# Kernel optimization log

Hardware: AMD Instinct MI355X
Metric: run time of the kernel (lower is better)

## Reference

```python
import jax, jax.numpy as jnp
import numpy as np

DIM = 640
M_SPATIAL = 100  # 10*10
BATCH = 64
EPS = 1e-5


def setup_inputs() -> dict:
    key = jax.random.key(0)
    kx, = jax.random.split(key, 1)
    x = jax.random.normal(kx, (BATCH, DIM, M_SPATIAL), dtype=jnp.float32)
    # temperature buffer: log(1 / (2 * H * W)) as in BDC.__init__
    t = jnp.log(1.0 / (2.0 * M_SPATIAL) * jnp.ones((1, 1), dtype=jnp.float32))
    return {"x": x, "t": t}


def reference(x, t):
    B, dim, M = x.shape
    # x_pow2 = x @ x^T  -> [B, dim, dim]
    x_pow2 = jnp.einsum('bim,bjm->bij', x, x)
    # I_M.bmm(x_pow2*I) broadcasts diag along rows; (x_pow2*I).bmm(I_M) along cols
    d = jnp.diagonal(x_pow2, axis1=1, axis2=2)  # [B, dim], squared norms
    dcov = d[:, :, None] + d[:, None, :] - 2.0 * x_pow2
    dcov = jnp.clip(dcov, 0.0)
    dcov = jnp.exp(t) * dcov
    dcov = jnp.sqrt(dcov + EPS)
    # double centering: dcov.bmm(I_M) = row sums broadcast, I_M.bmm(dcov) = col sums
    row_mean = jnp.sum(dcov, axis=2, keepdims=True) / dim          # [B, dim, 1]
    col_mean = jnp.sum(dcov, axis=1, keepdims=True) / dim          # [B, 1, dim]
    grand_mean = jnp.sum(dcov, axis=(1, 2), keepdims=True) / (dim * dim)
    bdc = dcov - row_mean - col_mean + grand_mean                   # [B, dim, dim]
    # Triuvec: upper triangle incl. diagonal, row-major order
    iu_r, iu_c = np.triu_indices(dim)
    return bdc[:, iu_r, iu_c]  # [B, dim*(dim+1)//2]
```

## Files before the change

kernel.cpp:

```cpp
#include <hip/hip_runtime.h>
#include <math.h>

#define BATCH 64
#define DIM   640
#define MSP   100
#define TILE  64
#define NT    10
#define NPAIR 55
#define PTRI  205120
#define EPSV  1e-5f

#define WS_D 0
#define WS_S 40960
#define WS_G 81920
#define XB_OFF 327936ull


typedef __attribute__((ext_vector_type(8))) short short8;
typedef __attribute__((ext_vector_type(4))) float f32x4;

__device__ __forceinline__ short f2bf(float f) {
    union { float f; unsigned u; } x; x.f = f;
    unsigned r = x.u + 0x7fffu + ((x.u >> 16) & 1u);
    return (short)(r >> 16);
}
__device__ __forceinline__ float bf2f(short h) {
    union { unsigned u; float f; } x; x.u = ((unsigned)(unsigned short)h) << 16;
    return x.f;
}

__device__ __forceinline__ void decode_pair(int u, int& ti, int& tj) {
    ti = 0;
    while (u >= NT - ti) { u -= NT - ti; ++ti; }
    tj = ti + u;
}

__device__ __forceinline__ void decode_block(int bid, int& b, int& ti, int& tj) {
    const int xcd = bid & 7;
    const int idx = bid >> 3;
    b = xcd + 8 * (idx & 7);
    decode_pair(idx >> 3, ti, tj);
}

__global__ __launch_bounds__(256) void k_prep(const float* __restrict__ x,
                                              float* __restrict__ ws) {
    short* xb = (short*)((char*)ws + XB_OFF);
    const int t = threadIdx.x;
    const int rr = t >> 4, c = t & 15;
    const int row = blockIdx.x * 16 + rr;
    const int k0 = c * 8;
    const float* src = x + (size_t)row * MSP;

    float v[8];
#pragma unroll
    for (int e = 0; e < 8; ++e) v[e] = 0.f;
    if (k0 <= 88) {
        float4 u0 = *(const float4*)(src + k0);
        float4 u1 = *(const float4*)(src + k0 + 4);
        v[0] = u0.x; v[1] = u0.y; v[2] = u0.z; v[3] = u0.w;
        v[4] = u1.x; v[5] = u1.y; v[6] = u1.z; v[7] = u1.w;
    } else if (k0 == 96) {
        float4 u0 = *(const float4*)(src + 96);
        v[0] = u0.x; v[1] = u0.y; v[2] = u0.z; v[3] = u0.w;
    }

    short8 h; float s = 0.f;
#pragma unroll
    for (int e = 0; e < 8; ++e) {
        short hb = f2bf(v[e]);
        float vr = bf2f(hb);
        s += vr * vr;
        h[e] = hb;
    }
    *(short8*)(xb + (size_t)blockIdx.x * 2048 + c * 128 + rr * 8) = h;

    s += __shfl_xor(s, 1); s += __shfl_xor(s, 2);
    s += __shfl_xor(s, 4); s += __shfl_xor(s, 8);
    if (c == 0) { ws[WS_D + row] = s; ws[WS_S + row] = 0.f; }
    if (blockIdx.x == 0 && t < BATCH) ws[WS_G + t] = 0.f;
}

__global__ __launch_bounds__(256) void k_sums(const float* __restrict__ tsc,
                                              float* __restrict__ ws) {
    __shared__ float sRow[TILE];
    __shared__ float sCol[TILE];

    int b, ti, tj;
    decode_block(blockIdx.x, b, ti, tj);
    const int i0 = ti * TILE, j0 = tj * TILE;
    const int tid = threadIdx.x;
    const short* xb = (const short*)((const char*)ws + XB_OFF);

    if (tid < TILE) { sRow[tid] = 0.f; sCol[tid] = 0.f; }

    const int wave = tid >> 6, lane = tid & 63;
    const int lm = lane & 15, lq = lane >> 4;
    const int r0 = (wave >> 1) * 32, c0 = (wave & 1) * 32;

    const short* pa = xb + (size_t)(b * 40 + ((i0 + r0) >> 4)) * 2048 + lq * 128 + lm * 8;
    const short* pb = xb + (size_t)(b * 40 + ((j0 + c0) >> 4)) * 2048 + lq * 128 + lm * 8;

    f32x4 acc[2][2] = {};
#pragma unroll
    for (int ks = 0; ks < 4; ++ks) {
        short8 a0 = *(const short8*)(pa + ks * 512);
        short8 a1 = *(const short8*)(pa + 2048 + ks * 512);
        short8 b0 = *(const short8*)(pb + ks * 512);
        short8 b1 = *(const short8*)(pb + 2048 + ks * 512);
        acc[0][0] = __builtin_amdgcn_mfma_f32_16x16x32_bf16(a0, b0, acc[0][0], 0, 0, 0);
        acc[0][1] = __builtin_amdgcn_mfma_f32_16x16x32_bf16(a0, b1, acc[0][1], 0, 0, 0);
        acc[1][0] = __builtin_amdgcn_mfma_f32_16x16x32_bf16(a1, b0, acc[1][0], 0, 0, 0);
        acc[1][1] = __builtin_amdgcn_mfma_f32_16x16x32_bf16(a1, b1, acc[1][1], 0, 0, 0);
    }

    const float scale = expf(tsc[0]);
    const float* dn = ws + WS_D + b * DIM;
    float di[2][4], dj[2];
#pragma unroll
    for (int a = 0; a < 2; ++a)
#pragma unroll
        for (int r = 0; r < 4; ++r) di[a][r] = dn[i0 + r0 + 16 * a + lq * 4 + r];
#pragma unroll
    for (int bb = 0; bb < 2; ++bb) dj[bb] = dn[j0 + c0 + 16 * bb + lm];

    float rp[2][4] = {}, cp[2] = {};
#pragma unroll
    for (int a = 0; a < 2; ++a)
#pragma unroll
        for (int bb = 0; bb < 2; ++bb)
#pragma unroll
            for (int p = 0; p < 2; ++p) {
                float d0 = di[a][2 * p]     + dj[bb];
                float d1 = di[a][2 * p + 1] + dj[bb];
                float v0 = __builtin_amdgcn_sqrtf(
                    fmaf(scale, fmaxf(fmaf(-2.f, acc[a][bb][2 * p],     d0), 0.f), EPSV));
                float v1 = __builtin_amdgcn_sqrtf(
                    fmaf(scale, fmaxf(fmaf(-2.f, acc[a][bb][2 * p + 1], d1), 0.f), EPSV));
                rp[a][2 * p] += v0; rp[a][2 * p + 1] += v1; cp[bb] += v0 + v1;
            }

    __syncthreads();
#pragma unroll
    for (int a = 0; a < 2; ++a)
#pragma unroll
        for (int r = 0; r < 4; ++r) {
            float v = rp[a][r];
            v += __shfl_xor(v, 1); v += __shfl_xor(v, 2);
            v += __shfl_xor(v, 4); v += __shfl_xor(v, 8);
            if (lm == 0) atomicAdd(&sRow[r0 + 16 * a + lq * 4 + r], v);
        }
#pragma unroll
    for (int bb = 0; bb < 2; ++bb) {
        float v = cp[bb];
        v += __shfl_xor(v, 16); v += __shfl_xor(v, 32);
        if (lq == 0) atomicAdd(&sCol[c0 + 16 * bb + lm], v);
    }
    __syncthreads();

    float* S = ws + WS_S + b * DIM;
    if (tid < TILE) {
        atomicAdd(&S[i0 + tid], sRow[tid]);
        if (ti != tj) atomicAdd(&S[j0 + tid], sCol[tid]);
        float gg = sRow[tid];
        gg += __shfl_xor(gg, 1);  gg += __shfl_xor(gg, 2);  gg += __shfl_xor(gg, 4);
        gg += __shfl_xor(gg, 8);  gg += __shfl_xor(gg, 16); gg += __shfl_xor(gg, 32);
        if (tid == 0) atomicAdd(&ws[WS_G + b], (ti == tj ? 1.f : 2.f) * gg);
    }
}

__global__ __launch_bounds__(256) void k_write(const float* __restrict__ tsc,
                                               const float* __restrict__ ws,
                                               float* __restrict__ out) {
    int b, ti, tj;
    decode_block(blockIdx.x, b, ti, tj);
    const int i0 = ti * TILE, j0 = tj * TILE;
    const int tid = threadIdx.x;
    const short* xb = (const short*)((const char*)ws + XB_OFF);

    const int wave = tid >> 6, lane = tid & 63;
    const int lm = lane & 15, lq = lane >> 4;
    const int r0 = (wave >> 1) * 32, c0 = (wave & 1) * 32;

    const short* pa = xb + (size_t)(b * 40 + ((i0 + r0) >> 4)) * 2048 + lq * 128 + lm * 8;
    const short* pb = xb + (size_t)(b * 40 + ((j0 + c0) >> 4)) * 2048 + lq * 128 + lm * 8;

    f32x4 acc[2][2] = {};
#pragma unroll
    for (int ks = 0; ks < 4; ++ks) {
        short8 a0 = *(const short8*)(pa + ks * 512);
        short8 a1 = *(const short8*)(pa + 2048 + ks * 512);
        short8 b0 = *(const short8*)(pb + ks * 512);
        short8 b1 = *(const short8*)(pb + 2048 + ks * 512);
        acc[0][0] = __builtin_amdgcn_mfma_f32_16x16x32_bf16(a0, b0, acc[0][0], 0, 0, 0);
        acc[0][1] = __builtin_amdgcn_mfma_f32_16x16x32_bf16(a0, b1, acc[0][1], 0, 0, 0);
        acc[1][0] = __builtin_amdgcn_mfma_f32_16x16x32_bf16(a1, b0, acc[1][0], 0, 0, 0);
        acc[1][1] = __builtin_amdgcn_mfma_f32_16x16x32_bf16(a1, b1, acc[1][1], 0, 0, 0);
    }

    const float scale = expf(tsc[0]);
    const float inv = 1.f / (float)DIM;
    const float g = ws[WS_G + b] * (inv * inv);
    const float* S  = ws + WS_S + b * DIM;
    const float* dn = ws + WS_D + b * DIM;

    float di[2][4], ai[2][4]; int ib[2][4];
#pragma unroll
    for (int a = 0; a < 2; ++a)
#pragma unroll
        for (int r = 0; r < 4; ++r) {
            int i = i0 + r0 + 16 * a + 4 * lq + r;
            di[a][r] = dn[i];
            ai[a][r] = g - S[i] * inv;
            ib[a][r] = i * DIM - (i * (i - 1)) / 2 - i;
        }
    float dj[2], bj[2]; int jj[2];
#pragma unroll
    for (int bb = 0; bb < 2; ++bb) {
        int j = j0 + c0 + 16 * bb + lm;
        jj[bb] = j; dj[bb] = dn[j]; bj[bb] = -S[j] * inv;
    }

    const bool offd = (ti != tj);
    float* outb = out + (size_t)b * PTRI;
#pragma unroll
    for (int a = 0; a < 2; ++a) {
        const int ibase = i0 + r0 + 16 * a + 4 * lq;
#pragma unroll
        for (int bb = 0; bb < 2; ++bb)
#pragma unroll
            for (int p = 0; p < 2; ++p) {
                const int r = 2 * p;
                float d0 = di[a][r]     + dj[bb];
                float d1 = di[a][r + 1] + dj[bb];
                float v0 = __builtin_amdgcn_sqrtf(
                    fmaf(scale, fmaxf(fmaf(-2.f, acc[a][bb][r],     d0), 0.f), EPSV));
                float v1 = __builtin_amdgcn_sqrtf(
                    fmaf(scale, fmaxf(fmaf(-2.f, acc[a][bb][r + 1], d1), 0.f), EPSV));
                if (offd || jj[bb] >= ibase + r)
                    outb[ib[a][r]     + jj[bb]] = v0 + ai[a][r]     + bj[bb];
                if (offd || jj[bb] >= ibase + r + 1)
                    outb[ib[a][r + 1] + jj[bb]] = v1 + ai[a][r + 1] + bj[bb];
            }
    }
}

extern "C" void kernel_launch(void* const* d_in, const int* in_sizes, int n_in,
                              void* d_out, int out_size, void* d_ws, size_t ws_size,
                              hipStream_t stream) {
    const float* x = (const float*)d_in[0];
    const float* t = (const float*)d_in[1];
    float* out = (float*)d_out;
    float* ws  = (float*)d_ws;

    k_prep <<<dim3(BATCH * DIM / 16),  256, 0, stream>>>(x, ws);
    k_sums <<<dim3(NPAIR * BATCH),     256, 0, stream>>>(t, ws);
    k_write<<<dim3(NPAIR * BATCH),     256, 0, stream>>>(t, ws, out);
}
```

Before: 123.4 us.

## Enlarge block tile to 128x128 and skip lower-triangle waves on diagonal tiles

Raises the per-block output tile from 64x64 to 128x128, so each wave computes a 64x64 sub-tile with a 4x4 grid of MFMA accumulators. The grid shrinks from 3520 to 960 blocks, and each A/B fragment is reused across four MFMAs instead of two. In the write kernel, diagonal tiles return early for waves that sit wholly below the diagonal, which skips their MFMA and sqrt work. The cost is higher register pressure from 16 accumulators, and only 960 blocks may leave part of the GPU idle or unevenly loaded.

```diff
diff --git a/kernel.cpp b/kernel.cpp
--- a/kernel.cpp
+++ b/kernel.cpp
@@ -4,9 +4,10 @@
 #define BATCH 64
 #define DIM   640
 #define MSP   100
-#define TILE  64
-#define NT    10
-#define NPAIR 55
+#define BT    128
+#define NT2   5
+#define NPAIR2 15
+#define NBLK2 960
 #define PTRI  205120
 #define EPSV  1e-5f
 
@@ -15,7 +16,6 @@
 #define WS_G 81920
 #define XB_OFF 327936ull
 
-
 typedef __attribute__((ext_vector_type(8))) short short8;
 typedef __attribute__((ext_vector_type(4))) float f32x4;
 
@@ -29,17 +29,17 @@
     return x.f;
 }
 
-__device__ __forceinline__ void decode_pair(int u, int& ti, int& tj) {
+__device__ __forceinline__ void decode_pair5(int u, int& ti, int& tj) {
     ti = 0;
-    while (u >= NT - ti) { u -= NT - ti; ++ti; }
+    while (u >= NT2 - ti) { u -= NT2 - ti; ++ti; }
     tj = ti + u;
 }
 
-__device__ __forceinline__ void decode_block(int bid, int& b, int& ti, int& tj) {
+__device__ __forceinline__ void decode_block128(int bid, int& b, int& ti, int& tj) {
     const int xcd = bid & 7;
     const int idx = bid >> 3;
     b = xcd + 8 * (idx & 7);
-    decode_pair(idx >> 3, ti, tj);
+    decode_pair5(idx >> 3, ti, tj);
 }
 
 __global__ __launch_bounds__(256) void k_prep(const float* __restrict__ x,
@@ -82,89 +82,87 @@
 
 __global__ __launch_bounds__(256) void k_sums(const float* __restrict__ tsc,
                                               float* __restrict__ ws) {
-    __shared__ float sRow[TILE];
-    __shared__ float sCol[TILE];
+    __shared__ float sRow[BT];
+    __shared__ float sCol[BT];
 
     int b, ti, tj;
-    decode_block(blockIdx.x, b, ti, tj);
-    const int i0 = ti * TILE, j0 = tj * TILE;
+    decode_block128(blockIdx.x, b, ti, tj);
+    const int i0 = ti * BT, j0 = tj * BT;
     const int tid = threadIdx.x;
     const short* xb = (const short*)((const char*)ws + XB_OFF);
 
-    if (tid < TILE) { sRow[tid] = 0.f; sCol[tid] = 0.f; }
+    if (tid < BT) { sRow[tid] = 0.f; sCol[tid] = 0.f; }
 
     const int wave = tid >> 6, lane = tid & 63;
     const int lm = lane & 15, lq = lane >> 4;
-    const int r0 = (wave >> 1) * 32, c0 = (wave & 1) * 32;
+    const int r0 = (wave >> 1) * 64, c0 = (wave & 1) * 64;
 
     const short* pa = xb + (size_t)(b * 40 + ((i0 + r0) >> 4)) * 2048 + lq * 128 + lm * 8;
     const short* pb = xb + (size_t)(b * 40 + ((j0 + c0) >> 4)) * 2048 + lq * 128 + lm * 8;
 
-    f32x4 acc[2][2] = {};
+    f32x4 acc[4][4] = {};
 #pragma unroll
     for (int ks = 0; ks < 4; ++ks) {
-        short8 a0 = *(const short8*)(pa + ks * 512);
-        short8 a1 = *(const short8*)(pa + 2048 + ks * 512);
-        short8 b0 = *(const short8*)(pb + ks * 512);
-        short8 b1 = *(const short8*)(pb + 2048 + ks * 512);
-        acc[0][0] = __builtin_amdgcn_mfma_f32_16x16x32_bf16(a0, b0, acc[0][0], 0, 0, 0);
-        acc[0][1] = __builtin_amdgcn_mfma_f32_16x16x32_bf16(a0, b1, acc[0][1], 0, 0, 0);
-        acc[1][0] = __builtin_amdgcn_mfma_f32_16x16x32_bf16(a1, b0, acc[1][0], 0, 0, 0);
-        acc[1][1] = __builtin_amdgcn_mfma_f32_16x16x32_bf16(a1, b1, acc[1][1], 0, 0, 0);
+        short8 af[4], bf[4];
+#pragma unroll
+        for (int m = 0; m < 4; ++m) af[m] = *(const short8*)(pa + m * 2048 + ks * 512);
+#pragma unroll
+        for (int n = 0; n < 4; ++n) bf[n] = *(const short8*)(pb + n * 2048 + ks * 512);
+#pragma unroll
+        for (int m = 0; m < 4; ++m)
+#pragma unroll
+            for (int n = 0; n < 4; ++n)
+                acc[m][n] = __builtin_amdgcn_mfma_f32_16x16x32_bf16(af[m], bf[n], acc[m][n], 0, 0, 0);
     }
 
     const float scale = expf(tsc[0]);
     const float* dn = ws + WS_D + b * DIM;
-    float di[2][4], dj[2];
-#pragma unroll
-    for (int a = 0; a < 2; ++a)
-#pragma unroll
-        for (int r = 0; r < 4; ++r) di[a][r] = dn[i0 + r0 + 16 * a + lq * 4 + r];
-#pragma unroll
-    for (int bb = 0; bb < 2; ++bb) dj[bb] = dn[j0 + c0 + 16 * bb + lm];
-
-    float rp[2][4] = {}, cp[2] = {};
-#pragma unroll
-    for (int a = 0; a < 2; ++a)
-#pragma unroll
-        for (int bb = 0; bb < 2; ++bb)
-#pragma unroll
-            for (int p = 0; p < 2; ++p) {
-                float d0 = di[a][2 * p]     + dj[bb];
-                float d1 = di[a][2 * p + 1] + dj[bb];
-                float v0 = __builtin_amdgcn_sqrtf(
-                    fmaf(scale, fmaxf(fmaf(-2.f, acc[a][bb][2 * p],     d0), 0.f), EPSV));
-                float v1 = __builtin_amdgcn_sqrtf(
-                    fmaf(scale, fmaxf(fmaf(-2.f, acc[a][bb][2 * p + 1], d1), 0.f), EPSV));
-                rp[a][2 * p] += v0; rp[a][2 * p + 1] += v1; cp[bb] += v0 + v1;
+    float dj[4];
+#pragma unroll
+    for (int n = 0; n < 4; ++n) dj[n] = dn[j0 + c0 + 16 * n + lm];
+
+    float rp[4][4] = {}, cp[4] = {};
+#pragma unroll
+    for (int m = 0; m < 4; ++m) {
+        float di_[4];
+#pragma unroll
+        for (int r = 0; r < 4; ++r) di_[r] = dn[i0 + r0 + 16 * m + 4 * lq + r];
+#pragma unroll
+        for (int n = 0; n < 4; ++n)
+#pragma unroll
+            for (int p = 0; p < 4; ++p) {
+                float v = __builtin_amdgcn_sqrtf(
+                    fmaf(scale, fmaxf(fmaf(-2.f, acc[m][n][p], di_[p] + dj[n]), 0.f), EPSV));
+                rp[m][p] += v; cp[n] += v;
             }
+    }
 
     __syncthreads();
 #pragma unroll
-    for (int a = 0; a < 2; ++a)
-#pragma unroll
-        for (int r = 0; r < 4; ++r) {
-            float v = rp[a][r];
+    for (int m = 0; m < 4; ++m)
+#pragma unroll
+        for (int p = 0; p < 4; ++p) {
+            float v = rp[m][p];
             v += __shfl_xor(v, 1); v += __shfl_xor(v, 2);
             v += __shfl_xor(v, 4); v += __shfl_xor(v, 8);
-            if (lm == 0) atomicAdd(&sRow[r0 + 16 * a + lq * 4 + r], v);
+            if (lm == 0) atomicAdd(&sRow[r0 + 16 * m + 4 * lq + p], v);
         }
 #pragma unroll
-    for (int bb = 0; bb < 2; ++bb) {
-        float v = cp[bb];
+    for (int n = 0; n < 4; ++n) {
+        float v = cp[n];
         v += __shfl_xor(v, 16); v += __shfl_xor(v, 32);
-        if (lq == 0) atomicAdd(&sCol[c0 + 16 * bb + lm], v);
+        if (lq == 0) atomicAdd(&sCol[c0 + 16 * n + lm], v);
     }
     __syncthreads();
 
     float* S = ws + WS_S + b * DIM;
-    if (tid < TILE) {
+    if (tid < BT) {
         atomicAdd(&S[i0 + tid], sRow[tid]);
         if (ti != tj) atomicAdd(&S[j0 + tid], sCol[tid]);
         float gg = sRow[tid];
         gg += __shfl_xor(gg, 1);  gg += __shfl_xor(gg, 2);  gg += __shfl_xor(gg, 4);
         gg += __shfl_xor(gg, 8);  gg += __shfl_xor(gg, 16); gg += __shfl_xor(gg, 32);
-        if (tid == 0) atomicAdd(&ws[WS_G + b], (ti == tj ? 1.f : 2.f) * gg);
+        if (lane == 0) atomicAdd(&ws[WS_G + b], (ti == tj ? 1.f : 2.f) * gg);
     }
 }
 
@@ -172,74 +170,71 @@
                                                const float* __restrict__ ws,
                                                float* __restrict__ out) {
     int b, ti, tj;
-    decode_block(blockIdx.x, b, ti, tj);
-    const int i0 = ti * TILE, j0 = tj * TILE;
+    decode_block128(blockIdx.x, b, ti, tj);
+    const int i0 = ti * BT, j0 = tj * BT;
     const int tid = threadIdx.x;
     const short* xb = (const short*)((const char*)ws + XB_OFF);
 
     const int wave = tid >> 6, lane = tid & 63;
     const int lm = lane & 15, lq = lane >> 4;
-    const int r0 = (wave >> 1) * 32, c0 = (wave & 1) * 32;
+    const int wr = wave >> 1, wc = wave & 1;
+    const int r0 = wr * 64, c0 = wc * 64;
+
+    const bool diag = (ti == tj);
+    if (diag && wr > wc) return;
+    const bool pred = diag && (wr == wc);
 
     const short* pa = xb + (size_t)(b * 40 + ((i0 + r0) >> 4)) * 2048 + lq * 128 + lm * 8;
     const short* pb = xb + (size_t)(b * 40 + ((j0 + c0) >> 4)) * 2048 + lq * 128 + lm * 8;
 
-    f32x4 acc[2][2] = {};
+    f32x4 acc[4][4] = {};
 #pragma unroll
     for (int ks = 0; ks < 4; ++ks) {
-        short8 a0 = *(const short8*)(pa + ks * 512);
-        short8 a1 = *(const short8*)(pa + 2048 + ks * 512);
-        short8 b0 = *(const short8*)(pb + ks * 512);
-        short8 b1 = *(const short8*)(pb + 2048 + ks * 512);
-        acc[0][0] = __builtin_amdgcn_mfma_f32_16x16x32_bf16(a0, b0, acc[0][0], 0, 0, 0);
-        acc[0][1] = __builtin_amdgcn_mfma_f32_16x16x32_bf16(a0, b1, acc[0][1], 0, 0, 0);
-        acc[1][0] = __builtin_amdgcn_mfma_f32_16x16x32_bf16(a1, b0, acc[1][0], 0, 0, 0);
-        acc[1][1] = __builtin_amdgcn_mfma_f32_16x16x32_bf16(a1, b1, acc[1][1], 0, 0, 0);
+        short8 af[4], bf[4];
+#pragma unroll
+        for (int m = 0; m < 4; ++m) af[m] = *(const short8*)(pa + m * 2048 + ks * 512);
+#pragma unroll
+        for (int n = 0; n < 4; ++n) bf[n] = *(const short8*)(pb + n * 2048 + ks * 512);
+#pragma unroll
+        for (int m = 0; m < 4; ++m)
+#pragma unroll
+            for (int n = 0; n < 4; ++n)
+                acc[m][n] = __builtin_amdgcn_mfma_f32_16x16x32_bf16(af[m], bf[n], acc[m][n], 0, 0, 0);
     }
 
     const float scale = expf(tsc[0]);
     const float inv = 1.f / (float)DIM;
-    const float g = ws[WS_G + b] * (inv * inv);
+    const float gmean = ws[WS_G + b] * (inv * inv);
     const float* S  = ws + WS_S + b * DIM;
     const float* dn = ws + WS_D + b * DIM;
 
-    float di[2][4], ai[2][4]; int ib[2][4];
-#pragma unroll
-    for (int a = 0; a < 2; ++a)
+    float dj[4], bj[4]; int jj[4];
+#pragma unroll
+    for (int n = 0; n < 4; ++n) {
+        int j = j0 + c0 + 16 * n + lm;
+        jj[n] = j; dj[n] = dn[j]; bj[n] = -S[j] * inv;
+    }
+
+    float* outb = out + (size_t)b * PTRI;
+#pragma unroll
+    for (int m = 0; m < 4; ++m) {
+        const int ibase = i0 + r0 + 16 * m + 4 * lq;
+        float di_[4], ai_[4]; int ib_[4];
 #pragma unroll
         for (int r = 0; r < 4; ++r) {
-            int i = i0 + r0 + 16 * a + 4 * lq + r;
-            di[a][r] = dn[i];
-            ai[a][r] = g - S[i] * inv;
-            ib[a][r] = i * DIM - (i * (i - 1)) / 2 - i;
+            int i = ibase + r;
+            di_[r] = dn[i];
+            ai_[r] = gmean - S[i] * inv;
+            ib_[r] = i * DIM - (i * (i - 1)) / 2 - i;
         }
-    float dj[2], bj[2]; int jj[2];
-#pragma unroll
-    for (int bb = 0; bb < 2; ++bb) {
-        int j = j0 + c0 + 16 * bb + lm;
-        jj[bb] = j; dj[bb] = dn[j]; bj[bb] = -S[j] * inv;
-    }
-
-    const bool offd = (ti != tj);
-    float* outb = out + (size_t)b * PTRI;
-#pragma unroll
-    for (int a = 0; a < 2; ++a) {
-        const int ibase = i0 + r0 + 16 * a + 4 * lq;
-#pragma unroll
-        for (int bb = 0; bb < 2; ++bb)
-#pragma unroll
-            for (int p = 0; p < 2; ++p) {
-                const int r = 2 * p;
-                float d0 = di[a][r]     + dj[bb];
-                float d1 = di[a][r + 1] + dj[bb];
-                float v0 = __builtin_amdgcn_sqrtf(
-                    fmaf(scale, fmaxf(fmaf(-2.f, acc[a][bb][r],     d0), 0.f), EPSV));
-                float v1 = __builtin_amdgcn_sqrtf(
-                    fmaf(scale, fmaxf(fmaf(-2.f, acc[a][bb][r + 1], d1), 0.f), EPSV));
-                if (offd || jj[bb] >= ibase + r)
-                    outb[ib[a][r]     + jj[bb]] = v0 + ai[a][r]     + bj[bb];
-                if (offd || jj[bb] >= ibase + r + 1)
-                    outb[ib[a][r + 1] + jj[bb]] = v1 + ai[a][r + 1] + bj[bb];
+#pragma unroll
+        for (int n = 0; n < 4; ++n)
+#pragma unroll
+            for (int p = 0; p < 4; ++p) {
+                float v = __builtin_amdgcn_sqrtf(
+                    fmaf(scale, fmaxf(fmaf(-2.f, acc[m][n][p], di_[p] + dj[n]), 0.f), EPSV));
+                if (!pred || jj[n] >= ibase + p)
+                    outb[ib_[p] + jj[n]] = v + ai_[p] + bj[n];
             }
     }
 }
@@ -252,7 +247,7 @@
     float* out = (float*)d_out;
     float* ws  = (float*)d_ws;
 
-    k_prep <<<dim3(BATCH * DIM / 16),  256, 0, stream>>>(x, ws);
-    k_sums <<<dim3(NPAIR * BATCH),     256, 0, stream>>>(t, ws);
-    k_write<<<dim3(NPAIR * BATCH),     256, 0, stream>>>(t, ws, out);
-}
+    k_prep <<<dim3(BATCH * DIM / 16), 256, 0, stream>>>(x, ws);
+    k_sums <<<dim3(NBLK2),            256, 0, stream>>>(t, ws);
+    k_write<<<dim3(NBLK2),            256, 0, stream>>>(t, ws, out);
+}
```

After: 124.5 us. Within noise of the previous version (+0.9%).
